# Optimization experiments

Hardware: AMD Instinct MI355X
Metric: run time of the kernel (lower is better)

Reference implementation:

```python
import jax, jax.numpy as jnp
import numpy as np
import math

B, N, DIM = 4, 2048, 512
HEADS, DIM_HEAD = 8, 64
INNER = HEADS * DIM_HEAD  # 512


def setup_inputs() -> dict:
    key = jax.random.key(0)
    ks = jax.random.split(key, 4)
    x = jax.random.normal(ks[0], (B, N, DIM), dtype=jnp.float32)
    # nn.Linear(dim, inner*4, bias=False): store as [dim, 4*inner] for x @ W
    w_qkvg = jax.random.normal(ks[1], (DIM, 4 * INNER), dtype=jnp.float32) * (1.0 / math.sqrt(DIM))
    sigma = jnp.full((1, HEADS, 1, 1), 1.92, dtype=jnp.float32)
    w_out = jax.random.normal(ks[2], (2 * INNER, DIM), dtype=jnp.float32) * (1.0 / math.sqrt(2 * INNER))
    b_out = jax.random.normal(ks[3], (DIM,), dtype=jnp.float32) * 0.01
    return {"x": x, "w_qkvg": w_qkvg, "sigma": sigma, "w_out": w_out, "b_out": b_out}


def reference(x, w_qkvg, sigma, w_out, b_out):
    b, n, d = x.shape
    h, dh = HEADS, DIM_HEAD
    scale = dh ** (-0.5)

    qkvg = x @ w_qkvg  # [b, n, 4*inner]
    q, k, vg, vsigma = jnp.split(qkvg, 4, axis=-1)

    def to_heads(t):  # [b, n, h*dh] -> [b, h, n, dh]
        return t.reshape(b, n, h, dh).transpose(0, 2, 1, 3)

    q, k, vg, vsigma = map(to_heads, (q, k, vg, vsigma))

    # --- softmax branch ---
    dots = jnp.einsum('bhid,bhjd->bhij', q, k) * scale  # [b, h, n, n]
    corr_g = jax.nn.softmax(dots, axis=-1)
    out_g = jnp.matmul(corr_g, vg)  # [b, h, n, dh]

    # --- Gaussian positional-mask branch ---
    pos = jnp.arange(1, n + 1, dtype=x.dtype)
    diffs = jnp.abs(pos[:, None] - pos[None, :])  # [n, n]
    inv_norm = 1.0 / (jnp.sqrt(jnp.asarray(2.0 * math.pi, x.dtype)) * sigma)  # [1, h, 1, 1]
    gm = inv_norm * jnp.exp(-(diffs ** 2)[None, None] / (2.0 * sigma ** 2))  # [1, h, n, n]
    corr_sigma = gm / gm.sum(-1, keepdims=True)
    out_s = jnp.matmul(corr_sigma, vsigma)  # broadcasts over batch -> [b, h, n, dh]

    out = jnp.concatenate([out_g, out_s], axis=-1)  # [b, h, n, 2*dh]
    out = out.transpose(0, 2, 1, 3).reshape(b, n, 2 * h * dh)
    return out @ w_out + b_out
```

## Files before the change

kernel.cpp:

```cpp
#include <hip/hip_runtime.h>

typedef _Float16 f16;
typedef __attribute__((ext_vector_type(8))) _Float16 f16x8;
typedef __attribute__((ext_vector_type(4))) _Float16 f16x4;
typedef __attribute__((ext_vector_type(4))) float f32x4;

#define B_ 4
#define N_ 2048
#define DIM_ 512
#define H_ 8
#define DH_ 64

__device__ __forceinline__ void gload16(const void* g, void* l) {
    __builtin_amdgcn_global_load_lds((const __attribute__((address_space(1))) void*)g,
                                     (__attribute__((address_space(3))) void*)l, 16, 0, 0);
}


__global__ __launch_bounds__(256) void cvt_f16_k8(const float* __restrict__ in,
                                                  f16* __restrict__ out, int n8) {
    int i = blockIdx.x * 256 + threadIdx.x;
    if (i < n8) {
        const float4 a = ((const float4*)in)[i * 2];
        const float4 b = ((const float4*)in)[i * 2 + 1];
        f16x8 o = {(f16)a.x, (f16)a.y, (f16)a.z, (f16)a.w,
                   (f16)b.x, (f16)b.y, (f16)b.z, (f16)b.w};
        ((f16x8*)out)[i] = o;
    }
}

__global__ __launch_bounds__(256) void transpose_cvt_k(const float* __restrict__ in,
                                                       f16* __restrict__ out, int K, int N) {
    __shared__ f16 tile[64][72];
    const int nbk = K >> 6;
    const int bk = blockIdx.x % nbk, bn = blockIdx.x / nbk;
    const int k0 = bk << 6, n0 = bn << 6;
    const int t = threadIdx.x;
    const int r = t >> 2, q = (t & 3) << 4;
#pragma unroll
    for (int u = 0; u < 4; u++) {
        const float4 v = *(const float4*)&in[(size_t)(k0 + r) * N + n0 + q + u * 4];
        tile[q + u * 4 + 0][r] = (f16)v.x;
        tile[q + u * 4 + 1][r] = (f16)v.y;
        tile[q + u * 4 + 2][r] = (f16)v.z;
        tile[q + u * 4 + 3][r] = (f16)v.w;
    }
    __syncthreads();
#pragma unroll
    for (int u = 0; u < 2; u++) {
        f16x8 o = *(const f16x8*)&tile[r][q + u * 8];
        *(f16x8*)&out[(size_t)(n0 + r) * K + k0 + q + u * 8] = o;
    }
}

template <int EPI>
__global__ __launch_bounds__(256) void gemm_bt(
    const f16* __restrict__ A, const f16* __restrict__ BT, int K, int N,
    f16* __restrict__ qb, f16* __restrict__ kb, f16* __restrict__ vbT,
    float* __restrict__ vsb, const float* __restrict__ bias, float* __restrict__ outp)
{
    __shared__ char sAb[16384];
    __shared__ char sBb[16384];
    const int tid = threadIdx.x;
    const int m0 = blockIdx.y * 128, n0 = blockIdx.x * 128;
    const int wave = tid >> 6, lane = tid & 63;
    const int wr = wave >> 1, wc = wave & 1;
    const int lr = lane & 15, lg = lane >> 4;

    f32x4 acc[4][4];
    const f32x4 zero = {0.f, 0.f, 0.f, 0.f};
#pragma unroll
    for (int i = 0; i < 4; i++)
#pragma unroll
        for (int j = 0; j < 4; j++) acc[i][j] = zero;

    const f16* srcA[4]; const f16* srcB[4];
    char* ldsA[4]; char* ldsB[4];
#pragma unroll
    for (int u = 0; u < 4; u++) {
        int row = wave * 8 + u * 32 + (lane >> 3);
        int e0 = ((lane & 7) ^ (row & 7)) << 3;
        srcA[u] = A + (size_t)(m0 + row) * K + e0;
        srcB[u] = BT + (size_t)(n0 + row) * K + e0;
        ldsA[u] = sAb + wave * 1024 + u * 4096;
        ldsB[u] = sBb + wave * 1024 + u * 4096;
    }

    const int swz = (lr & 7) << 4;
    for (int kt = 0; kt < K; kt += 64) {
#pragma unroll
        for (int u = 0; u < 4; u++) {
            gload16(srcA[u], ldsA[u]);
            gload16(srcB[u], ldsB[u]);
            srcA[u] += 64; srcB[u] += 64;
        }
        __syncthreads();
#pragma unroll
        for (int half = 0; half < 2; half++) {
            f16x8 af[4], bf[4];
#pragma unroll
            for (int i = 0; i < 4; i++) {
                int R = wr * 64 + i * 16 + lr;
                af[i] = *(const f16x8*)(sAb + R * 128 + (((half << 6) | (lg << 4)) ^ swz));
            }
#pragma unroll
            for (int j = 0; j < 4; j++) {
                int R = wc * 64 + j * 16 + lr;
                bf[j] = *(const f16x8*)(sBb + R * 128 + (((half << 6) | (lg << 4)) ^ swz));
            }
#pragma unroll
            for (int i = 0; i < 4; i++)
#pragma unroll
                for (int j = 0; j < 4; j++)
                    acc[i][j] = __builtin_amdgcn_mfma_f32_16x16x32_f16(af[i], bf[j], acc[i][j], 0, 0, 0);
        }
        __syncthreads();
    }

#pragma unroll
    for (int i = 0; i < 4; i++) {
#pragma unroll
        for (int j = 0; j < 4; j++) {
            int col = n0 + wc * 64 + j * 16 + lr;
            int row0 = m0 + wr * 64 + i * 16 + lg * 4;
            if (EPI == 0) {
                int sec = col >> 9, cc = col & 511;
                int h = cc >> 6, d = cc & 63;
                int b = row0 >> 11, ns = row0 & 2047;
                if (sec == 2) {
                    f16x4 o;
#pragma unroll
                    for (int r = 0; r < 4; r++) o[r] = (f16)acc[i][j][r];
                    *(f16x4*)&vbT[((size_t)(b * H_ + h) * DH_ + d) * N_ + ns] = o;
                } else if (sec == 0) {
#pragma unroll
                    for (int r = 0; r < 4; r++)
                        qb[((size_t)(b * H_ + h) * N_ + ns + r) * DH_ + d] = (f16)(acc[i][j][r] * 0.1803368801f);
                } else if (sec == 1) {
#pragma unroll
                    for (int r = 0; r < 4; r++)
                        kb[((size_t)(b * H_ + h) * N_ + ns + r) * DH_ + d] = (f16)acc[i][j][r];
                } else {
#pragma unroll
                    for (int r = 0; r < 4; r++)
                        vsb[((size_t)(b * H_ + h) * N_ + ns + r) * DH_ + d] = acc[i][j][r];
                }
            } else {
#pragma unroll
                for (int r = 0; r < 4; r++)
                    outp[(size_t)(row0 + r) * N + col] = acc[i][j][r] + bias[col];
            }
        }
    }
}

__global__ __launch_bounds__(256) void gemm_small(
    const f16* __restrict__ A, const f16* __restrict__ BT, int K, int N,
    const float* __restrict__ bias, float* __restrict__ outp)
{
    __shared__ char sAb[8192];
    __shared__ char sBb[8192];
    const int tid = threadIdx.x;
    const int m0 = blockIdx.y * 64, n0 = blockIdx.x * 64;
    const int wave = tid >> 6, lane = tid & 63;
    const int wr = wave >> 1, wc = wave & 1;
    const int lr = lane & 15, lg = lane >> 4;

    f32x4 acc[2][2];
    const f32x4 zero = {0.f, 0.f, 0.f, 0.f};
#pragma unroll
    for (int i = 0; i < 2; i++)
#pragma unroll
        for (int j = 0; j < 2; j++) acc[i][j] = zero;

    const f16* srcA[2]; const f16* srcB[2];
    char* ldsA[2]; char* ldsB[2];
#pragma unroll
    for (int u = 0; u < 2; u++) {
        int row = wave * 8 + u * 32 + (lane >> 3);
        int e0 = ((lane & 7) ^ (row & 7)) << 3;
        srcA[u] = A + (size_t)(m0 + row) * K + e0;
        srcB[u] = BT + (size_t)(n0 + row) * K + e0;
        ldsA[u] = sAb + wave * 1024 + u * 4096;
        ldsB[u] = sBb + wave * 1024 + u * 4096;
    }

    const int swz = (lr & 7) << 4;
    for (int kt = 0; kt < K; kt += 64) {
#pragma unroll
        for (int u = 0; u < 2; u++) {
            gload16(srcA[u], ldsA[u]);
            gload16(srcB[u], ldsB[u]);
            srcA[u] += 64; srcB[u] += 64;
        }
        __syncthreads();
#pragma unroll
        for (int half = 0; half < 2; half++) {
            f16x8 af[2], bf[2];
#pragma unroll
            for (int i = 0; i < 2; i++) {
                int R = wr * 32 + i * 16 + lr;
                af[i] = *(const f16x8*)(sAb + R * 128 + (((half << 6) | (lg << 4)) ^ swz));
            }
#pragma unroll
            for (int j = 0; j < 2; j++) {
                int R = wc * 32 + j * 16 + lr;
                bf[j] = *(const f16x8*)(sBb + R * 128 + (((half << 6) | (lg << 4)) ^ swz));
            }
#pragma unroll
            for (int i = 0; i < 2; i++)
#pragma unroll
                for (int j = 0; j < 2; j++)
                    acc[i][j] = __builtin_amdgcn_mfma_f32_16x16x32_f16(af[i], bf[j], acc[i][j], 0, 0, 0);
        }
        __syncthreads();
    }

#pragma unroll
    for (int i = 0; i < 2; i++)
#pragma unroll
        for (int j = 0; j < 2; j++) {
            int col = n0 + wc * 32 + j * 16 + lr;
            int row0 = m0 + wr * 32 + i * 16 + lg * 4;
#pragma unroll
            for (int r = 0; r < 4; r++)
                outp[(size_t)(row0 + r) * N + col] = acc[i][j][r] + bias[col];
        }
}

__global__ __launch_bounds__(256) void attn_k(
    const f16* __restrict__ qb, const f16* __restrict__ kb, const f16* __restrict__ vbT,
    f16* __restrict__ cat)
{
    __shared__ char sKbf[3 * 8192];
    __shared__ char sVbf[2 * 8192];
    const int tid = threadIdx.x;
    const int bid0 = blockIdx.x;
    const int obid = (bid0 & 7) * 128 + (bid0 >> 3);
    const int bh = obid >> 5, qblk = obid & 31;
    const int b = bh >> 3, h = bh & 7;
    const int wave = tid >> 6, lane = tid & 63;
    const int lr = lane & 15, lg = lane >> 4;

    const size_t base = (size_t)bh * N_ * DH_;
    const int qrow = qblk * 64 + wave * 16 + lr;
    const f16x8 qf0 = *(const f16x8*)&qb[base + (size_t)qrow * DH_ + lg * 8];
    const f16x8 qf1 = *(const f16x8*)&qb[base + (size_t)qrow * DH_ + 32 + lg * 8];

    const f16* kq[2]; const f16* vq[2];
#pragma unroll
    for (int u = 0; u < 2; u++) {
        int row = wave * 8 + u * 32 + (lane >> 3);
        int e0 = ((lane & 7) ^ (row & 7)) << 3;
        kq[u] = kb + base + (size_t)row * 64 + e0;
        vq[u] = vbT + base + (size_t)row * 2048 + e0;
    }
    char* const ldsKw = sKbf + wave * 1024;
    char* const ldsVw = sVbf + wave * 1024;

    f32x4 Ot[4], lacc;
    const f32x4 zero = {0.f, 0.f, 0.f, 0.f};
#pragma unroll
    for (int dt = 0; dt < 4; dt++) Ot[dt] = zero;
    lacc = zero;
    const f16x4 onesA = {(f16)1.f, (f16)1.f, (f16)1.f, (f16)1.f};

    const int swz = (lr & 7) << 4;

#pragma unroll
    for (int u = 0; u < 2; u++) gload16(kq[u], ldsKw + u * 4096);
#pragma unroll
    for (int u = 0; u < 2; u++) gload16(vq[u], ldsVw + u * 4096);
#pragma unroll
    for (int u = 0; u < 2; u++) gload16(kq[u] + 4096, ldsKw + 8192 + u * 4096);

    int kcur = 0;
    int kpre = 2;
    for (int t = 0; t < 32; t++) {
        __builtin_amdgcn_s_barrier();
        {
            const int vtn = (t + 1) & 31, ktn = (t + 2) & 31;
            char* vdst = ldsVw + ((t + 1) & 1) * 8192;
            char* kdst = ldsKw + kpre * 8192;
#pragma unroll
            for (int u = 0; u < 2; u++) gload16(vq[u] + vtn * 64, vdst + u * 4096);
#pragma unroll
            for (int u = 0; u < 2; u++) gload16(kq[u] + ktn * 4096, kdst + u * 4096);
        }
        asm volatile("s_waitcnt vmcnt(6)" ::: "memory");
        __builtin_amdgcn_sched_barrier(0);

        const char* Kb = sKbf + kcur * 8192;
        const char* Vb = sVbf + (t & 1) * 8192;

        f32x4 st[4];
        __builtin_amdgcn_s_setprio(1);
#pragma unroll
        for (int ct = 0; ct < 4; ct++) {
            int row = ct * 16 + lr;
            f16x8 kf0 = *(const f16x8*)(Kb + (((row << 7) | (lg << 4)) ^ swz));
            f16x8 kf1 = *(const f16x8*)(Kb + (((row << 7) | 64 | (lg << 4)) ^ swz));
            f32x4 s = __builtin_amdgcn_mfma_f32_16x16x32_f16(kf0, qf0, zero, 0, 0, 0);
            st[ct]   = __builtin_amdgcn_mfma_f32_16x16x32_f16(kf1, qf1, s, 0, 0, 0);
        }
        __builtin_amdgcn_s_setprio(0);

        f16x4 pp[4];
#pragma unroll
        for (int ct = 0; ct < 4; ct++)
#pragma unroll
            for (int r = 0; r < 4; r++)
                pp[ct][r] = (f16)__builtin_amdgcn_exp2f(st[ct][r]);

        __builtin_amdgcn_s_setprio(1);
#pragma unroll
        for (int ct = 0; ct < 4; ct++)
            lacc = __builtin_amdgcn_mfma_f32_16x16x16f16(onesA, pp[ct], lacc, 0, 0, 0);
#pragma unroll
        for (int dt = 0; dt < 4; dt++) {
            int row = dt * 16 + lr;
#pragma unroll
            for (int ct = 0; ct < 4; ct++) {
                f16x4 vt = *(const f16x4*)(Vb + (((row << 7) | (ct * 32) | (lg << 3)) ^ swz));
                Ot[dt] = __builtin_amdgcn_mfma_f32_16x16x16f16(vt, pp[ct], Ot[dt], 0, 0, 0);
            }
        }
        __builtin_amdgcn_s_setprio(0);

        kcur = (kcur == 2) ? 0 : kcur + 1;
        kpre = (kpre == 2) ? 0 : kpre + 1;
    }

    float inv = 1.0f / lacc[0];
#pragma unroll
    for (int dt = 0; dt < 4; dt++) {
        f16x4 o;
#pragma unroll
        for (int r = 0; r < 4; r++) o[r] = (f16)(Ot[dt][r] * inv);
        *(f16x4*)&cat[((size_t)(b * N_ + qrow)) * 1024 + h * 128 + dt * 16 + lg * 4] = o;
    }
}

__global__ __launch_bounds__(256) void gauss_k(
    const float* __restrict__ vsb, const float* __restrict__ sigma, f16* __restrict__ cat)
{
    const int tid = threadIdx.x;
    const int bh = blockIdx.y, b = bh >> 3, h = bh & 7;
    const int i0 = blockIdx.x * 64;
    const int wv = tid >> 6, d = tid & 63;
    const float sig = sigma[h];
    const float c = 0.72134752f / (sig * sig);

    float wt[17];
#pragma unroll
    for (int o = 0; o <= 16; o++) wt[o] = __builtin_amdgcn_exp2f(-(float)(o * o) * c);
    float wfull = wt[0];
#pragma unroll
    for (int o = 1; o <= 16; o++) wfull += 2.f * wt[o];
    const float inv_wfull = 1.0f / wfull;

    const size_t base = (size_t)bh * N_ * DH_;
    const int r0 = i0 + wv * 16 - 16;
    float v[48];
#pragma unroll
    for (int k = 0; k < 48; k++) {
        int r = r0 + k; r = r < 0 ? 0 : (r > N_ - 1 ? N_ - 1 : r);
        v[k] = vsb[base + (size_t)r * DH_ + d];
    }

#pragma unroll
    for (int it = 0; it < 16; it++) {
        int i = i0 + wv * 16 + it;
        float acc = 0.f;
        if (i >= 16 && i <= N_ - 17) {
#pragma unroll
            for (int o = -16; o <= 16; o++)
                acc += wt[o < 0 ? -o : o] * v[16 + it + o];
            acc *= inv_wfull;
        } else {
            float ws = 0.f;
#pragma unroll
            for (int o = -16; o <= 16; o++) {
                int j = i + o;
                if (j >= 0 && j <= N_ - 1) {
                    float w = wt[o < 0 ? -o : o];
                    ws += w;
                    acc += w * v[16 + it + o];
                }
            }
            acc /= ws;
        }
        cat[((size_t)(b * N_ + i)) * 1024 + h * 128 + 64 + d] = (f16)acc;
    }
}


extern "C" void kernel_launch(void* const* d_in, const int* in_sizes, int n_in,
                              void* d_out, int out_size, void* d_ws, size_t ws_size,
                              hipStream_t stream) {
    const float* x      = (const float*)d_in[0];
    const float* w_qkvg = (const float*)d_in[1];
    const float* sigma  = (const float*)d_in[2];
    const float* w_out  = (const float*)d_in[3];
    const float* b_out  = (const float*)d_in[4];
    float* out = (float*)d_out;
    char* ws = (char*)d_ws;

    const size_t MB = 1048576;
    f16*   x16 = (f16*)(ws);
    f16*   wqT = (f16*)(ws + 8 * MB);
    f16*   woT = (f16*)(ws + 10 * MB);
    f16*   qb  = (f16*)(ws + 11 * MB);
    f16*   kb  = (f16*)(ws + 19 * MB);
    f16*   vbT = (f16*)(ws + 27 * MB);
    float* vsb = (float*)(ws + 35 * MB);
    f16*   cat = (f16*)(ws + 51 * MB);
    if (ws_size < 67 * MB) return;

    cvt_f16_k8<<<2048, 256, 0, stream>>>(x, x16, B_ * N_ * DIM_ / 8);
    transpose_cvt_k<<<256, 256, 0, stream>>>(w_qkvg, wqT, 512, 2048);
    transpose_cvt_k<<<128, 256, 0, stream>>>(w_out, woT, 1024, 512);

    gemm_bt<0><<<dim3(16, 64), 256, 0, stream>>>(x16, wqT, 512, 2048,
                                                 qb, kb, vbT, vsb, nullptr, nullptr);

    attn_k<<<1024, 256, 0, stream>>>(qb, kb, vbT, cat);
    gauss_k<<<dim3(32, 32), 256, 0, stream>>>(vsb, sigma, cat);

    gemm_small<<<dim3(8, 128), 256, 0, stream>>>(cat, woT, 1024, 512, b_out, out);
}
```

Before: 135.2 us.

## Process two 16-row query tiles per wave in attention kernel

Each wave now handles 32 query rows instead of 16, so every K and V fragment read from LDS feeds two sets of MFMAs. The grid is halved to 512 blocks of 128 query rows each. This halves the global-to-LDS K/V traffic and the LDS reads per unit of work, and gives each wave more independent MFMAs between loads. In exchange it roughly doubles accumulator register use and leaves fewer blocks to fill 256 CUs, which can lower occupancy.

```diff
diff --git a/kernel.cpp b/kernel.cpp
--- a/kernel.cpp
+++ b/kernel.cpp
@@ -236,16 +236,19 @@
     __shared__ char sVbf[2 * 8192];
     const int tid = threadIdx.x;
     const int bid0 = blockIdx.x;
-    const int obid = (bid0 & 7) * 128 + (bid0 >> 3);
-    const int bh = obid >> 5, qblk = obid & 31;
+    const int obid = (bid0 & 7) * 64 + (bid0 >> 3);
+    const int bh = obid >> 4, qblk = obid & 15;
     const int b = bh >> 3, h = bh & 7;
     const int wave = tid >> 6, lane = tid & 63;
     const int lr = lane & 15, lg = lane >> 4;
 
     const size_t base = (size_t)bh * N_ * DH_;
-    const int qrow = qblk * 64 + wave * 16 + lr;
-    const f16x8 qf0 = *(const f16x8*)&qb[base + (size_t)qrow * DH_ + lg * 8];
-    const f16x8 qf1 = *(const f16x8*)&qb[base + (size_t)qrow * DH_ + 32 + lg * 8];
+    const int qrow_a = qblk * 128 + wave * 32 + lr;
+    const int qrow_b = qrow_a + 16;
+    const f16x8 qfa0 = *(const f16x8*)&qb[base + (size_t)qrow_a * DH_ + lg * 8];
+    const f16x8 qfa1 = *(const f16x8*)&qb[base + (size_t)qrow_a * DH_ + 32 + lg * 8];
+    const f16x8 qfb0 = *(const f16x8*)&qb[base + (size_t)qrow_b * DH_ + lg * 8];
+    const f16x8 qfb1 = *(const f16x8*)&qb[base + (size_t)qrow_b * DH_ + 32 + lg * 8];
 
     const f16* kq[2]; const f16* vq[2];
 #pragma unroll
@@ -258,11 +261,11 @@
     char* const ldsKw = sKbf + wave * 1024;
     char* const ldsVw = sVbf + wave * 1024;
 
-    f32x4 Ot[4], lacc;
+    f32x4 Ota[4], Otb[4], lacc_a, lacc_b;
     const f32x4 zero = {0.f, 0.f, 0.f, 0.f};
 #pragma unroll
-    for (int dt = 0; dt < 4; dt++) Ot[dt] = zero;
-    lacc = zero;
+    for (int dt = 0; dt < 4; dt++) { Ota[dt] = zero; Otb[dt] = zero; }
+    lacc_a = zero; lacc_b = zero;
     const f16x4 onesA = {(f16)1.f, (f16)1.f, (f16)1.f, (f16)1.f};
 
     const int swz = (lr & 7) << 4;
@@ -293,36 +296,43 @@
         const char* Kb = sKbf + kcur * 8192;
         const char* Vb = sVbf + (t & 1) * 8192;
 
-        f32x4 st[4];
+        f32x4 sta[4], stb[4];
         __builtin_amdgcn_s_setprio(1);
 #pragma unroll
         for (int ct = 0; ct < 4; ct++) {
             int row = ct * 16 + lr;
             f16x8 kf0 = *(const f16x8*)(Kb + (((row << 7) | (lg << 4)) ^ swz));
             f16x8 kf1 = *(const f16x8*)(Kb + (((row << 7) | 64 | (lg << 4)) ^ swz));
-            f32x4 s = __builtin_amdgcn_mfma_f32_16x16x32_f16(kf0, qf0, zero, 0, 0, 0);
-            st[ct]   = __builtin_amdgcn_mfma_f32_16x16x32_f16(kf1, qf1, s, 0, 0, 0);
+            f32x4 sa = __builtin_amdgcn_mfma_f32_16x16x32_f16(kf0, qfa0, zero, 0, 0, 0);
+            sta[ct]  = __builtin_amdgcn_mfma_f32_16x16x32_f16(kf1, qfa1, sa, 0, 0, 0);
+            f32x4 sb = __builtin_amdgcn_mfma_f32_16x16x32_f16(kf0, qfb0, zero, 0, 0, 0);
+            stb[ct]  = __builtin_amdgcn_mfma_f32_16x16x32_f16(kf1, qfb1, sb, 0, 0, 0);
         }
         __builtin_amdgcn_s_setprio(0);
 
-        f16x4 pp[4];
+        f16x4 ppa[4], ppb[4];
 #pragma unroll
         for (int ct = 0; ct < 4; ct++)
 #pragma unroll
-            for (int r = 0; r < 4; r++)
-                pp[ct][r] = (f16)__builtin_amdgcn_exp2f(st[ct][r]);
+            for (int r = 0; r < 4; r++) {
+                ppa[ct][r] = (f16)__builtin_amdgcn_exp2f(sta[ct][r]);
+                ppb[ct][r] = (f16)__builtin_amdgcn_exp2f(stb[ct][r]);
+            }
 
         __builtin_amdgcn_s_setprio(1);
 #pragma unroll
-        for (int ct = 0; ct < 4; ct++)
-            lacc = __builtin_amdgcn_mfma_f32_16x16x16f16(onesA, pp[ct], lacc, 0, 0, 0);
+        for (int ct = 0; ct < 4; ct++) {
+            lacc_a = __builtin_amdgcn_mfma_f32_16x16x16f16(onesA, ppa[ct], lacc_a, 0, 0, 0);
+            lacc_b = __builtin_amdgcn_mfma_f32_16x16x16f16(onesA, ppb[ct], lacc_b, 0, 0, 0);
+        }
 #pragma unroll
         for (int dt = 0; dt < 4; dt++) {
             int row = dt * 16 + lr;
 #pragma unroll
             for (int ct = 0; ct < 4; ct++) {
                 f16x4 vt = *(const f16x4*)(Vb + (((row << 7) | (ct * 32) | (lg << 3)) ^ swz));
-                Ot[dt] = __builtin_amdgcn_mfma_f32_16x16x16f16(vt, pp[ct], Ot[dt], 0, 0, 0);
+                Ota[dt] = __builtin_amdgcn_mfma_f32_16x16x16f16(vt, ppa[ct], Ota[dt], 0, 0, 0);
+                Otb[dt] = __builtin_amdgcn_mfma_f32_16x16x16f16(vt, ppb[ct], Otb[dt], 0, 0, 0);
             }
         }
         __builtin_amdgcn_s_setprio(0);
@@ -331,13 +341,18 @@
         kpre = (kpre == 2) ? 0 : kpre + 1;
     }
 
-    float inv = 1.0f / lacc[0];
+    float inv_a = 1.0f / lacc_a[0];
+    float inv_b = 1.0f / lacc_b[0];
 #pragma unroll
     for (int dt = 0; dt < 4; dt++) {
-        f16x4 o;
-#pragma unroll
-        for (int r = 0; r < 4; r++) o[r] = (f16)(Ot[dt][r] * inv);
-        *(f16x4*)&cat[((size_t)(b * N_ + qrow)) * 1024 + h * 128 + dt * 16 + lg * 4] = o;
+        f16x4 oa, ob;
+#pragma unroll
+        for (int r = 0; r < 4; r++) {
+            oa[r] = (f16)(Ota[dt][r] * inv_a);
+            ob[r] = (f16)(Otb[dt][r] * inv_b);
+        }
+        *(f16x4*)&cat[((size_t)(b * N_ + qrow_a)) * 1024 + h * 128 + dt * 16 + lg * 4] = oa;
+        *(f16x4*)&cat[((size_t)(b * N_ + qrow_b)) * 1024 + h * 128 + dt * 16 + lg * 4] = ob;
     }
 }
 
@@ -424,7 +439,7 @@
     gemm_bt<0><<<dim3(16, 64), 256, 0, stream>>>(x16, wqT, 512, 2048,
                                                  qb, kb, vbT, vsb, nullptr, nullptr);
 
-    attn_k<<<1024, 256, 0, stream>>>(qb, kb, vbT, cat);
+    attn_k<<<512, 256, 0, stream>>>(qb, kb, vbT, cat);
     gauss_k<<<dim3(32, 32), 256, 0, stream>>>(vsb, sigma, cat);
 
     gemm_small<<<dim3(8, 128), 256, 0, stream>>>(cat, woT, 1024, 512, b_out, out);
```

Result: no change. 134.4 us (-0.6%).

## Switch attention kernel to 32x32x16 MFMA with 128-row query tiles

Applied to the files above, without the earlier changes.

Reworks the softmax-attention kernel so each wave handles 32 query rows using 32x32x16 MFMA instructions instead of 16x16 ones, which doubles the query tile per block and halves the grid to 512 blocks. The row-sum is now accumulated in registers with VALU adds plus a cross-half shuffle, replacing the ones-matrix MFMA. P is repacked into the B-operand layout via lane-xor-32 shuffles. This aims to reuse each K/V tile loaded into LDS across more queries and to issue fewer, larger MFMAs. In exchange it adds shuffle overhead and register pressure, and the smaller grid may under-occupy the GPU's compute units.

```diff
diff --git a/kernel.cpp b/kernel.cpp
--- a/kernel.cpp
+++ b/kernel.cpp
@@ -4,6 +4,9 @@
 typedef __attribute__((ext_vector_type(8))) _Float16 f16x8;
 typedef __attribute__((ext_vector_type(4))) _Float16 f16x4;
 typedef __attribute__((ext_vector_type(4))) float f32x4;
+typedef __attribute__((ext_vector_type(16))) float f32x16;
+typedef __attribute__((ext_vector_type(2))) unsigned int u32x2;
+typedef __attribute__((ext_vector_type(4))) unsigned int u32x4;
 
 #define B_ 4
 #define N_ 2048
@@ -236,16 +239,18 @@
     __shared__ char sVbf[2 * 8192];
     const int tid = threadIdx.x;
     const int bid0 = blockIdx.x;
-    const int obid = (bid0 & 7) * 128 + (bid0 >> 3);
-    const int bh = obid >> 5, qblk = obid & 31;
-    const int b = bh >> 3, h = bh & 7;
+    const int obid = (bid0 & 7) * 64 + (bid0 >> 3);
+    const int bh = obid >> 4, qblk = obid & 15;
+    const int b = bh >> 3, h_head = bh & 7;
     const int wave = tid >> 6, lane = tid & 63;
-    const int lr = lane & 15, lg = lane >> 4;
+    const int l31 = lane & 31, hh = lane >> 5;
 
     const size_t base = (size_t)bh * N_ * DH_;
-    const int qrow = qblk * 64 + wave * 16 + lr;
-    const f16x8 qf0 = *(const f16x8*)&qb[base + (size_t)qrow * DH_ + lg * 8];
-    const f16x8 qf1 = *(const f16x8*)&qb[base + (size_t)qrow * DH_ + 32 + lg * 8];
+    const int qrow = qblk * 128 + wave * 32 + l31;
+    f16x8 qf[4];
+#pragma unroll
+    for (int c = 0; c < 4; c++)
+        qf[c] = *(const f16x8*)&qb[base + (size_t)qrow * DH_ + c * 16 + hh * 8];
 
     const f16* kq[2]; const f16* vq[2];
 #pragma unroll
@@ -258,14 +263,10 @@
     char* const ldsKw = sKbf + wave * 1024;
     char* const ldsVw = sVbf + wave * 1024;
 
-    f32x4 Ot[4], lacc;
-    const f32x4 zero = {0.f, 0.f, 0.f, 0.f};
-#pragma unroll
-    for (int dt = 0; dt < 4; dt++) Ot[dt] = zero;
-    lacc = zero;
-    const f16x4 onesA = {(f16)1.f, (f16)1.f, (f16)1.f, (f16)1.f};
-
-    const int swz = (lr & 7) << 4;
+    f32x16 Ot0 = 0.f, Ot1 = 0.f;
+    float l_run = 0.f;
+
+    const int swz = (lane & 7) << 4;
 
 #pragma unroll
     for (int u = 0; u < 2; u++) gload16(kq[u], ldsKw + u * 4096);
@@ -274,8 +275,7 @@
 #pragma unroll
     for (int u = 0; u < 2; u++) gload16(kq[u] + 4096, ldsKw + 8192 + u * 4096);
 
-    int kcur = 0;
-    int kpre = 2;
+    int kcur = 0, kpre = 2;
     for (int t = 0; t < 32; t++) {
         __builtin_amdgcn_s_barrier();
         {
@@ -293,51 +293,83 @@
         const char* Kb = sKbf + kcur * 8192;
         const char* Vb = sVbf + (t & 1) * 8192;
 
-        f32x4 st[4];
+        f32x16 st[2];
         __builtin_amdgcn_s_setprio(1);
 #pragma unroll
-        for (int ct = 0; ct < 4; ct++) {
-            int row = ct * 16 + lr;
-            f16x8 kf0 = *(const f16x8*)(Kb + (((row << 7) | (lg << 4)) ^ swz));
-            f16x8 kf1 = *(const f16x8*)(Kb + (((row << 7) | 64 | (lg << 4)) ^ swz));
-            f32x4 s = __builtin_amdgcn_mfma_f32_16x16x32_f16(kf0, qf0, zero, 0, 0, 0);
-            st[ct]   = __builtin_amdgcn_mfma_f32_16x16x32_f16(kf1, qf1, s, 0, 0, 0);
+        for (int kt = 0; kt < 2; kt++) {
+            int row = kt * 32 + l31;
+            f32x16 s = 0.f;
+#pragma unroll
+            for (int c = 0; c < 4; c++) {
+                f16x8 kf = *(const f16x8*)(Kb + (((row << 7) | (c << 5) | (hh << 4)) ^ swz));
+                s = __builtin_amdgcn_mfma_f32_32x32x16_f16(kf, qf[c], s, 0, 0, 0);
+            }
+            st[kt] = s;
         }
         __builtin_amdgcn_s_setprio(0);
 
-        f16x4 pp[4];
-#pragma unroll
-        for (int ct = 0; ct < 4; ct++)
-#pragma unroll
-            for (int r = 0; r < 4; r++)
-                pp[ct][r] = (f16)__builtin_amdgcn_exp2f(st[ct][r]);
-
-        __builtin_amdgcn_s_setprio(1);
-#pragma unroll
-        for (int ct = 0; ct < 4; ct++)
-            lacc = __builtin_amdgcn_mfma_f32_16x16x16f16(onesA, pp[ct], lacc, 0, 0, 0);
-#pragma unroll
-        for (int dt = 0; dt < 4; dt++) {
-            int row = dt * 16 + lr;
-#pragma unroll
-            for (int ct = 0; ct < 4; ct++) {
-                f16x4 vt = *(const f16x4*)(Vb + (((row << 7) | (ct * 32) | (lg << 3)) ^ swz));
-                Ot[dt] = __builtin_amdgcn_mfma_f32_16x16x16f16(vt, pp[ct], Ot[dt], 0, 0, 0);
-            }
-        }
-        __builtin_amdgcn_s_setprio(0);
+        u32x2 qw[2][4];
+#pragma unroll
+        for (int kt = 0; kt < 2; kt++) {
+            float p[16];
+#pragma unroll
+            for (int i = 0; i < 16; i++) p[i] = __builtin_amdgcn_exp2f(st[kt][i]);
+            l_run += ((p[0] + p[1]) + (p[2] + p[3])) + ((p[4] + p[5]) + (p[6] + p[7]))
+                   + ((p[8] + p[9]) + (p[10] + p[11])) + ((p[12] + p[13]) + (p[14] + p[15]));
+#pragma unroll
+            for (int rq = 0; rq < 4; rq++) {
+                f16x4 qd = {(f16)p[4 * rq], (f16)p[4 * rq + 1], (f16)p[4 * rq + 2], (f16)p[4 * rq + 3]};
+                qw[kt][rq] = __builtin_bit_cast(u32x2, qd);
+            }
+        }
+
+#pragma unroll
+        for (int kt = 0; kt < 2; kt++) {
+#pragma unroll
+            for (int c2 = 0; c2 < 2; c2++) {
+                unsigned a0 = qw[kt][2 * c2][0],     a1 = qw[kt][2 * c2][1];
+                unsigned b0 = qw[kt][2 * c2 + 1][0], b1 = qw[kt][2 * c2 + 1][1];
+                unsigned ca0 = (unsigned)__shfl_xor((int)a0, 32);
+                unsigned ca1 = (unsigned)__shfl_xor((int)a1, 32);
+                unsigned cb0 = (unsigned)__shfl_xor((int)b0, 32);
+                unsigned cb1 = (unsigned)__shfl_xor((int)b1, 32);
+                u32x4 bw;
+                bw[0] = hh ? cb0 : a0;
+                bw[1] = hh ? cb1 : a1;
+                bw[2] = hh ? b0 : ca0;
+                bw[3] = hh ? b1 : ca1;
+                f16x8 bf = __builtin_bit_cast(f16x8, bw);
+                const int cg = kt * 2 + c2;
+                __builtin_amdgcn_s_setprio(1);
+                {
+                    int row0 = l31;
+                    f16x8 vf0 = *(const f16x8*)(Vb + (((row0 << 7) | (cg << 5) | (hh << 4)) ^ swz));
+                    Ot0 = __builtin_amdgcn_mfma_f32_32x32x16_f16(vf0, bf, Ot0, 0, 0, 0);
+                    int row1 = 32 + l31;
+                    f16x8 vf1 = *(const f16x8*)(Vb + (((row1 << 7) | (cg << 5) | (hh << 4)) ^ swz));
+                    Ot1 = __builtin_amdgcn_mfma_f32_32x32x16_f16(vf1, bf, Ot1, 0, 0, 0);
+                }
+                __builtin_amdgcn_s_setprio(0);
+            }
+        }
 
         kcur = (kcur == 2) ? 0 : kcur + 1;
         kpre = (kpre == 2) ? 0 : kpre + 1;
     }
 
-    float inv = 1.0f / lacc[0];
-#pragma unroll
-    for (int dt = 0; dt < 4; dt++) {
-        f16x4 o;
-#pragma unroll
-        for (int r = 0; r < 4; r++) o[r] = (f16)(Ot[dt][r] * inv);
-        *(f16x4*)&cat[((size_t)(b * N_ + qrow)) * 1024 + h * 128 + dt * 16 + lg * 4] = o;
+    l_run += __shfl_xor(l_run, 32);
+    float inv = 1.0f / l_run;
+#pragma unroll
+    for (int dt = 0; dt < 2; dt++) {
+        const f32x16& O = dt ? Ot1 : Ot0;
+#pragma unroll
+        for (int rq = 0; rq < 4; rq++) {
+            f16x4 o;
+#pragma unroll
+            for (int r = 0; r < 4; r++) o[r] = (f16)(O[4 * rq + r] * inv);
+            int d0 = dt * 32 + rq * 8 + hh * 4;
+            *(f16x4*)&cat[((size_t)(b * N_ + qrow)) * 1024 + h_head * 128 + d0] = o;
+        }
     }
 }
 
@@ -424,7 +456,7 @@
     gemm_bt<0><<<dim3(16, 64), 256, 0, stream>>>(x16, wqT, 512, 2048,
                                                  qb, kb, vbT, vsb, nullptr, nullptr);
 
-    attn_k<<<1024, 256, 0, stream>>>(qb, kb, vbT, cat);
+    attn_k<<<512, 256, 0, stream>>>(qb, kb, vbT, cat);
     gauss_k<<<dim3(32, 32), 256, 0, stream>>>(vsb, sigma, cat);
 
     gemm_small<<<dim3(8, 128), 256, 0, stream>>>(cat, woT, 1024, 512, b_out, out);
```

Result: no change. 136.5 us (+1.0%).
